# Optimization experiments

Measured on AMD Instinct MI355X. Metric: run time of the kernel, lower is better.

## Reference

```python
import jax, jax.numpy as jnp
import numpy as np

FIND_T = 0.5      # FIND_THRESHOLD
IOU_T = 0.5       # IOU_THRESHOLD
DET_T = 0.5       # DETECT_THRESHOLD
DATA_W = 416.0
DATA_H = 416.0
TOPK = 512        # fixed candidate budget for jit-compatible NMS


def _decode(out, anchors, s1, s2, case1, case2):
    # out: (B, 3*(5+C), S, S) raw head.  Faithful to get_index_and_bias +
    # get_true_position, but dense: invalid cells carried with a mask.
    B, _, S, _ = out.shape
    o = jnp.transpose(out, (0, 2, 3, 1)).reshape(B, S, S, 3, -1)  # (B,y,x,a,5+C)
    obj = jax.nn.sigmoid(o[..., 0])
    valid = obj > FIND_T
    grid = jnp.arange(S, dtype=out.dtype)
    cx = (grid[None, None, :, None] + o[..., 1]) * s1 / case1   # x index is dim 2
    cy = (grid[None, :, None, None] + o[..., 2]) * s2 / case2   # y index is dim 1
    w = jnp.exp(o[..., 3]) * anchors[:, 0] / case1              # anchors bcast over a
    h = jnp.exp(o[..., 4]) * anchors[:, 1] / case2
    cprob = jax.nn.softmax(o[..., 5:], axis=-1)
    p = obj * jnp.max(cprob, axis=-1)
    cls = jnp.argmax(cprob, axis=-1).astype(out.dtype)
    boxes = jnp.stack([p, cx, cy, w, h, cls], axis=-1).reshape(-1, 6)
    return boxes, valid.reshape(-1)


def _pairwise_iou(b):
    # b: (K,4) in (cx,cy,w,h); vectorized form of compute_iou for all pairs
    x1 = b[:, 0] - b[:, 2] / 2
    y1 = b[:, 1] - b[:, 3] / 2
    x2 = x1 + b[:, 2]
    y2 = y1 + b[:, 3]
    iw = jnp.clip(jnp.minimum(x2[:, None], x2[None, :]) - jnp.maximum(x1[:, None], x1[None, :]), 0.0)
    ih = jnp.clip(jnp.minimum(y2[:, None], y2[None, :]) - jnp.maximum(y1[:, None], y1[None, :]), 0.0)
    inter = iw * ih
    area = (x2 - x1) * (y2 - y1)
    return inter / (area[:, None] + area[None, :] - inter)


def _detect(out13, out26, out52, anchors13, anchors26, anchors52, case1, case2):
    b13, v13 = _decode(out13, anchors13, DATA_W / 13, DATA_H / 13, case1, case2)
    b26, v26 = _decode(out26, anchors26, DATA_W / 26, DATA_H / 26, case1, case2)
    b52, v52 = _decode(out52, anchors52, DATA_W / 52, DATA_H / 52, case1, case2)
    boxes = jnp.concatenate([b13, b26, b52], axis=0)
    valid = jnp.concatenate([v13, v26, v52], axis=0)

    # sort by score (descending) via fixed-size top-k over valid candidates
    score = jnp.where(valid, boxes[:, 0], -1.0)
    top_scores, idx = jax.lax.top_k(score, TOPK)
    cand = boxes[idx]                      # (K,6) sorted desc by p
    alive0 = top_scores > 0.0              # passed find-threshold
    max_p = jnp.max(jnp.where(alive0, cand[:, 0], 0.0))
    alive0 = alive0 & (cand[:, 0] > DET_T * max_p)

    iou = _pairwise_iou(cand[:, 1:5])
    same_cls = cand[:, 5][:, None] == cand[:, 5][None, :]
    # original drops all same-class boxes after a keep, and cross-class boxes
    # with iou >= threshold
    suppress_pair = same_cls | (iou >= IOU_T)
    rng = jnp.arange(TOPK)

    def body(i, state):
        suppressed, keep = state
        active = jnp.logical_not(suppressed[i])
        keep = keep.at[i].set(active)
        sup_row = active & suppress_pair[i] & (rng > i)
        return suppressed | sup_row, keep

    suppressed0 = jnp.logical_not(alive0)
    _, keep = jax.lax.fori_loop(0, TOPK, body, (suppressed0, jnp.zeros(TOPK, dtype=bool)))
    boxes_out = cand * keep[:, None].astype(cand.dtype)
    return boxes_out, keep


def setup_inputs() -> dict:
    key = jax.random.key(0)
    k1, k2, k3 = jax.random.split(key, 3)
    B, C = 32, 3 * (5 + 80)
    return {
        "out13": jax.random.normal(k1, (B, C, 13, 13), dtype=jnp.float32),
        "out26": jax.random.normal(k2, (B, C, 26, 26), dtype=jnp.float32),
        "out52": jax.random.normal(k3, (B, C, 52, 52), dtype=jnp.float32),
        "anchors13": jnp.array([[116, 90], [156, 198], [373, 326]], dtype=jnp.float32),
        "anchors26": jnp.array([[30, 61], [62, 45], [59, 119]], dtype=jnp.float32),
        "anchors52": jnp.array([[10, 13], [16, 30], [33, 23]], dtype=jnp.float32),
        "case1": jnp.float32(1.0),
        "case2": jnp.float32(1.0),
    }


def reference(out13, out26, out52, anchors13, anchors26, anchors52, case1, case2):
    return _detect(out13, out26, out52, anchors13, anchors26, anchors52, case1, case2)
```

## Files before the change

### kernel.cpp

```cpp
#include <hip/hip_runtime.h>
#include <math.h>


#define NCAND 340704
#define NCELL 113568
#define CAP   4096
#define HELEM 16
#define CELEM 4

#define OFF13 0
#define OFF26 16224
#define OFF52 81120
#define CELLS13 5408
#define CELLS26 21632

#define FIND_T 0.5f
#define IOU_T  0.5f
#define DET_T  0.5f
#define DATA_W 416.0f

#define WS_SCORES   0u
#define WS_CHIST    1362816u
#define WS_FHIST    1363840u
#define WS_COUNTER  1364864u
#define WS_KEYS     1364872u
#define WS_SKEYS    1397640u
#define WS_CAND6    1401736u
#define WS_VALID    1414024u
#define WS_MATRIX   1416072u

__device__ __forceinline__ unsigned int fmono(float f) {
    unsigned int u = __float_as_uint(f);
    return (u & 0x80000000u) ? ~u : (u | 0x80000000u);
}

__device__ int pick_bin256(unsigned int h, unsigned int need, unsigned int* above) {
    __shared__ unsigned int S[256];
    __shared__ int best; __shared__ unsigned int abv;
    int t = threadIdx.x;
    S[t] = h;
    __syncthreads();
    for (int off = 1; off < 256; off <<= 1) {
        unsigned int v = (t + off < 256) ? S[t + off] : 0u;
        __syncthreads();
        S[t] += v;
        __syncthreads();
    }
    if (t == 0) { best = 0; abv = 0; }
    __syncthreads();
    if (S[t] >= need && (t == 255 || S[t + 1] < need)) { best = t; abv = S[t] - h; }
    __syncthreads();
    if (above) *above = abv;
    return best;
}

__global__ void k_scores(const float* __restrict__ in13,
                         const float* __restrict__ in26,
                         const float* __restrict__ in52,
                         float* __restrict__ scores) {
    int cell = blockIdx.x * blockDim.x + threadIdx.x;
    if (cell >= NCELL) return;

    const float* in; int SS, b, s, candOff;
    if (cell < CELLS13) {
        in = in13; SS = 169; int l = cell;
        b = l / 169; s = l - b * 169; candOff = OFF13 + l * 3;
    } else if (cell < CELLS13 + CELLS26) {
        in = in26; SS = 676; int l = cell - CELLS13;
        b = l / 676; s = l - b * 676; candOff = OFF26 + l * 3;
    } else {
        in = in52; SS = 2704; int l = cell - (CELLS13 + CELLS26);
        b = l / 2704; s = l - b * 2704; candOff = OFF52 + l * 3;
    }

    for (int a = 0; a < 3; ++a) {
        const float* base = in + (size_t)(b * 255 + a * 85) * (size_t)SS + s;
        float o0  = base[0];
        float obj = 1.0f / (1.0f + expf(-o0));
        float vals[80];
#pragma unroll
        for (int c = 0; c < 80; ++c) vals[c] = base[(size_t)(5 + c) * (size_t)SS];
        float m = vals[0];
#pragma unroll
        for (int c = 1; c < 80; ++c) m = fmaxf(m, vals[c]);
        float sum = 0.0f;
#pragma unroll
        for (int c = 0; c < 80; ++c) sum += expf(vals[c] - m);
        float p = obj * (1.0f / sum);
        scores[candOff + a] = (obj > FIND_T) ? p : -1.0f;
    }
}

__global__ void k_hist_coarse(const float* __restrict__ scores,
                              unsigned int* __restrict__ chist) {
    __shared__ unsigned int h[256];
    int t = threadIdx.x;
    h[t] = 0;
    __syncthreads();
    int base = blockIdx.x * 256 * HELEM;
    for (int e = 0; e < HELEM; ++e) {
        int i = base + e * 256 + t;
        if (i < NCAND) atomicAdd(&h[fmono(scores[i]) >> 24], 1u);
    }
    __syncthreads();
    if (h[t]) atomicAdd(&chist[t], h[t]);
}

__global__ void k_hist_fine(const float* __restrict__ scores,
                            const unsigned int* __restrict__ chist,
                            unsigned int* __restrict__ fhist) {
    __shared__ unsigned int h[256];
    int t = threadIdx.x;
    unsigned int c = (unsigned int)pick_bin256(chist[t], 512u, 0);
    h[t] = 0;
    __syncthreads();
    int base = blockIdx.x * 256 * HELEM;
    for (int e = 0; e < HELEM; ++e) {
        int i = base + e * 256 + t;
        if (i < NCAND) {
            unsigned int mono = fmono(scores[i]);
            if ((mono >> 24) == c) atomicAdd(&h[(mono >> 16) & 0xFFu], 1u);
        }
    }
    __syncthreads();
    if (h[t]) atomicAdd(&fhist[t], h[t]);
}

__global__ void k_compact(const float* __restrict__ scores,
                          const unsigned int* __restrict__ chist,
                          const unsigned int* __restrict__ fhist,
                          unsigned int* __restrict__ counter,
                          unsigned long long* __restrict__ keys) {
    int t = threadIdx.x;
    unsigned int above;
    unsigned int c = (unsigned int)pick_bin256(chist[t], 512u, &above);
    unsigned int f = (unsigned int)pick_bin256(fhist[t], 512u - above, 0);
    unsigned int T = (c << 8) | f;

    int base = blockIdx.x * 256 * CELEM;
    for (int e = 0; e < CELEM; ++e) {
        int i = base + e * 256 + t;
        if (i < NCAND) {
            unsigned int mono = fmono(scores[i]);
            if ((mono >> 16) >= T) {
                unsigned int pos = atomicAdd(counter, 1u);
                if (pos < CAP)
                    keys[pos] = ((unsigned long long)mono << 32) |
                                (unsigned int)(~(unsigned int)i);
            }
        }
    }
}

__global__ void k_sort(const unsigned long long* __restrict__ keysg,
                       const unsigned int* __restrict__ counter,
                       unsigned long long* __restrict__ sorted) {
    __shared__ unsigned long long keys[CAP];
    int tid = threadIdx.x;
    unsigned int n = *counter; if (n > CAP) n = CAP;
    for (int t = tid; t < CAP; t += 1024)
        keys[t] = (t < (int)n) ? keysg[t] : 0ULL;
    __syncthreads();

    int sz = 1024;
    while ((unsigned)sz < n) sz <<= 1;

    for (int k = 2; k <= sz; k <<= 1) {
        for (int j = k >> 1; j > 0; j >>= 1) {
            for (int t = tid; t < (sz >> 1); t += 1024) {
                int i   = ((t & ~(j - 1)) << 1) | (t & (j - 1));
                int ixj = i | j;
                bool dir = ((i & k) == 0);
                unsigned long long x = keys[i], y = keys[ixj];
                if ((x < y) == dir) { keys[i] = y; keys[ixj] = x; }
            }
            __syncthreads();
        }
    }
    if (tid < 512) sorted[tid] = keys[tid];
}

__global__ void k_decode(const unsigned long long* __restrict__ sorted,
                         const float* __restrict__ in13,
                         const float* __restrict__ in26,
                         const float* __restrict__ in52,
                         const float* __restrict__ a13,
                         const float* __restrict__ a26,
                         const float* __restrict__ a52,
                         const float* __restrict__ c1p,
                         const float* __restrict__ c2p,
                         float* __restrict__ cand6,
                         unsigned int* __restrict__ valid) {
    int w = blockIdx.x * (blockDim.x >> 6) + (threadIdx.x >> 6);
    int lane = threadIdx.x & 63;
    if (w >= 512) return;

    unsigned long long key = sorted[w];
    int g = (int)(~(unsigned int)(key & 0xFFFFFFFFULL));

    const float* in; const float* anch; int S, SS, l;
    if (g < OFF26)      { in = in13; anch = a13; S = 13; SS = 169;  l = g - OFF13; }
    else if (g < OFF52) { in = in26; anch = a26; S = 26; SS = 676;  l = g - OFF26; }
    else                { in = in52; anch = a52; S = 52; SS = 2704; l = g - OFF52; }
    int a = l % 3; int cell = l / 3;
    int b = cell / SS; int s = cell - b * SS;
    int y = s / S; int x = s - y * S;

    const float* base = in + (size_t)(b * 255 + a * 85) * (size_t)SS + s;

    float hdr  = (lane < 5) ? base[(size_t)lane * (size_t)SS] : 0.0f;
    float val0 = base[(size_t)(5 + lane) * (size_t)SS];
    float val1 = (lane < 16) ? base[(size_t)(69 + lane) * (size_t)SS] : -INFINITY;

    float mx = fmaxf(val0, val1);
#pragma unroll
    for (int o = 32; o; o >>= 1) mx = fmaxf(mx, __shfl_xor(mx, o, 64));
    int i0 = (val0 == mx) ? lane : 1000;
    int i1 = (val1 == mx) ? lane + 64 : 1000;
    int li = i0 < i1 ? i0 : i1;
#pragma unroll
    for (int o = 32; o; o >>= 1) { int v = __shfl_xor(li, o, 64); li = v < li ? v : li; }
    float e = expf(val0 - mx) + ((lane < 16) ? expf(val1 - mx) : 0.0f);
#pragma unroll
    for (int o = 32; o; o >>= 1) e += __shfl_xor(e, o, 64);

    float o0 = __shfl(hdr, 0, 64);
    float o1 = __shfl(hdr, 1, 64);
    float o2 = __shfl(hdr, 2, 64);
    float o3 = __shfl(hdr, 3, 64);
    float o4 = __shfl(hdr, 4, 64);

    if (lane == 0) {
        float c1 = *c1p, c2 = *c2p;
        float obj = 1.0f / (1.0f + expf(-o0));
        float p = obj * (1.0f / e);
        float sgrid = DATA_W / (float)S;
        cand6[w * 6 + 0] = p;
        cand6[w * 6 + 1] = ((float)x + o1) * sgrid / c1;
        cand6[w * 6 + 2] = ((float)y + o2) * sgrid / c2;
        cand6[w * 6 + 3] = expf(o3) * anch[a * 2 + 0] / c1;
        cand6[w * 6 + 4] = expf(o4) * anch[a * 2 + 1] / c2;
        cand6[w * 6 + 5] = (float)li;
        valid[w] = ((unsigned int)(key >> 32) > 0x80000000u) ? 1u : 0u;
    }
}

__global__ void k_pairs(const float* __restrict__ cand6,
                        unsigned char* __restrict__ matrix) {
    int t = blockIdx.x * blockDim.x + threadIdx.x;
    if (t >= 512 * 64) return;
    int i = t >> 6, l = t & 63;
    float cxi = cand6[i * 6 + 1], cyi = cand6[i * 6 + 2];
    float wi  = cand6[i * 6 + 3], hi  = cand6[i * 6 + 4];
    float ci  = cand6[i * 6 + 5];
    float x1i = cxi - wi / 2.0f, y1i = cyi - hi / 2.0f;
    float x2i = x1i + wi,        y2i = y1i + hi;
    float ai  = (x2i - x1i) * (y2i - y1i);

    unsigned int byte = 0;
#pragma unroll
    for (int b = 0; b < 8; ++b) {
        int j = l * 8 + b;
        if (j > i) {
            float cxj = cand6[j * 6 + 1], cyj = cand6[j * 6 + 2];
            float wj  = cand6[j * 6 + 3], hj  = cand6[j * 6 + 4];
            float cj  = cand6[j * 6 + 5];
            bool sup = (ci == cj);
            if (!sup) {
                float x1j = cxj - wj / 2.0f, y1j = cyj - hj / 2.0f;
                float x2j = x1j + wj,        y2j = y1j + hj;
                float aj  = (x2j - x1j) * (y2j - y1j);
                float iw = fminf(x2i, x2j) - fmaxf(x1i, x1j); iw = fmaxf(iw, 0.0f);
                float ih = fminf(y2i, y2j) - fmaxf(y1i, y1j); ih = fmaxf(ih, 0.0f);
                float inter = iw * ih;
                float iou = inter / (ai + aj - inter);
                sup = (iou >= IOU_T);
            }
            byte |= ((unsigned int)sup) << b;
        }
    }
    matrix[i * 64 + l] = (unsigned char)byte;
}

__global__ void k_nms(const unsigned char* __restrict__ matrix,
                      const unsigned int* __restrict__ valid,
                      const float* __restrict__ cand6,
                      float* __restrict__ out) {
    __shared__ uint4 mbuf[2048];
    const unsigned char* m = (const unsigned char*)mbuf;
    int lane = threadIdx.x;

    const uint4* src = (const uint4*)matrix;
    for (int t = lane; t < 2048; t += 64) mbuf[t] = src[t];

    float maxp = valid[0] ? cand6[0] : 0.0f;

    unsigned int state = 0;
#pragma unroll
    for (int b = 0; b < 8; ++b) {
        int r = lane * 8 + b;
        bool alive = valid[r] && (cand6[r * 6] > DET_T * maxp);
        if (!alive) state |= 1u << b;
    }
    __syncthreads();

    unsigned int keepmask = 0;
    for (int i = 0; i < 512; ++i) {
        int srcl = i >> 3, bit = i & 7;
        unsigned int sb = (unsigned int)__shfl((int)state, srcl, 64);
        bool active = ((sb >> bit) & 1u) == 0u;
        if (lane == srcl && active) keepmask |= 1u << bit;
        if (active) state |= (unsigned int)m[i * 64 + lane];
    }

#pragma unroll
    for (int b = 0; b < 8; ++b) {
        int r = lane * 8 + b;
        float k = ((keepmask >> b) & 1u) ? 1.0f : 0.0f;
        for (int c = 0; c < 6; ++c) out[r * 6 + c] = cand6[r * 6 + c] * k;
        out[512 * 6 + r] = k;
    }
}

extern "C" void kernel_launch(void* const* d_in, const int* in_sizes, int n_in,
                              void* d_out, int out_size, void* d_ws, size_t ws_size,
                              hipStream_t stream) {
    (void)in_sizes; (void)n_in; (void)out_size; (void)ws_size;
    const float* in13 = (const float*)d_in[0];
    const float* in26 = (const float*)d_in[1];
    const float* in52 = (const float*)d_in[2];
    const float* a13  = (const float*)d_in[3];
    const float* a26  = (const float*)d_in[4];
    const float* a52  = (const float*)d_in[5];
    const float* c1p  = (const float*)d_in[6];
    const float* c2p  = (const float*)d_in[7];

    char* wsb = (char*)d_ws;
    float* scores             = (float*)(wsb + WS_SCORES);
    unsigned int* chist       = (unsigned int*)(wsb + WS_CHIST);
    unsigned int* fhist       = (unsigned int*)(wsb + WS_FHIST);
    unsigned int* counter     = (unsigned int*)(wsb + WS_COUNTER);
    unsigned long long* keys  = (unsigned long long*)(wsb + WS_KEYS);
    unsigned long long* skeys = (unsigned long long*)(wsb + WS_SKEYS);
    float* cand6              = (float*)(wsb + WS_CAND6);
    unsigned int* valid       = (unsigned int*)(wsb + WS_VALID);
    unsigned char* matrix     = (unsigned char*)(wsb + WS_MATRIX);

    hipMemsetAsync(wsb + WS_CHIST, 0, 1024 + 1024 + 8, stream);

    const int hblocks = (NCAND + 256 * HELEM - 1) / (256 * HELEM);
    const int cblocks = (NCAND + 256 * CELEM - 1) / (256 * CELEM);

    k_scores<<<(NCELL + 255) / 256, 256, 0, stream>>>(in13, in26, in52, scores);
    k_hist_coarse<<<hblocks, 256, 0, stream>>>(scores, chist);
    k_hist_fine<<<hblocks, 256, 0, stream>>>(scores, chist, fhist);
    k_compact<<<cblocks, 256, 0, stream>>>(scores, chist, fhist, counter, keys);
    k_sort<<<1, 1024, 0, stream>>>(keys, counter, skeys);
    k_decode<<<128, 256, 0, stream>>>(skeys, in13, in26, in52,
                                      a13, a26, a52, c1p, c2p, cand6, valid);
    k_pairs<<<128, 256, 0, stream>>>(cand6, matrix);
    k_nms<<<1, 64, 0, stream>>>(matrix, valid, cand6, (float*)d_out);
}
```

Before: 263.4 us.

## Fuse score computation with coarse histogram and pairwise IoU with NMS

The score kernel now builds the coarse 256-bin histogram in shared memory as it writes each score, so the separate pass that re-reads all scores goes away. The pairwise IoU matrix kernel and the serial NMS kernel are merged into one 1024-thread block that keeps candidates and the suppression matrix in LDS. This drops two launches and the global round trip for the matrix. In exchange, the IoU work now runs on a single workgroup instead of 128 blocks, so it has far less parallelism.

```diff
diff --git a/kernel.cpp b/kernel.cpp
--- a/kernel.cpp
+++ b/kernel.cpp
@@ -27,7 +27,6 @@
 #define WS_SKEYS    1397640u
 #define WS_CAND6    1401736u
 #define WS_VALID    1414024u
-#define WS_MATRIX   1416072u
 
 __device__ __forceinline__ unsigned int fmono(float f) {
     unsigned int u = __float_as_uint(f);
@@ -54,53 +53,48 @@
     return best;
 }
 
-__global__ void k_scores(const float* __restrict__ in13,
-                         const float* __restrict__ in26,
-                         const float* __restrict__ in52,
-                         float* __restrict__ scores) {
-    int cell = blockIdx.x * blockDim.x + threadIdx.x;
-    if (cell >= NCELL) return;
-
-    const float* in; int SS, b, s, candOff;
-    if (cell < CELLS13) {
-        in = in13; SS = 169; int l = cell;
-        b = l / 169; s = l - b * 169; candOff = OFF13 + l * 3;
-    } else if (cell < CELLS13 + CELLS26) {
-        in = in26; SS = 676; int l = cell - CELLS13;
-        b = l / 676; s = l - b * 676; candOff = OFF26 + l * 3;
-    } else {
-        in = in52; SS = 2704; int l = cell - (CELLS13 + CELLS26);
-        b = l / 2704; s = l - b * 2704; candOff = OFF52 + l * 3;
-    }
-
-    for (int a = 0; a < 3; ++a) {
-        const float* base = in + (size_t)(b * 255 + a * 85) * (size_t)SS + s;
-        float o0  = base[0];
-        float obj = 1.0f / (1.0f + expf(-o0));
-        float vals[80];
-#pragma unroll
-        for (int c = 0; c < 80; ++c) vals[c] = base[(size_t)(5 + c) * (size_t)SS];
-        float m = vals[0];
-#pragma unroll
-        for (int c = 1; c < 80; ++c) m = fmaxf(m, vals[c]);
-        float sum = 0.0f;
-#pragma unroll
-        for (int c = 0; c < 80; ++c) sum += expf(vals[c] - m);
-        float p = obj * (1.0f / sum);
-        scores[candOff + a] = (obj > FIND_T) ? p : -1.0f;
-    }
-}
-
-__global__ void k_hist_coarse(const float* __restrict__ scores,
+__global__ void k_scores_hist(const float* __restrict__ in13,
+                              const float* __restrict__ in26,
+                              const float* __restrict__ in52,
+                              float* __restrict__ scores,
                               unsigned int* __restrict__ chist) {
     __shared__ unsigned int h[256];
     int t = threadIdx.x;
     h[t] = 0;
     __syncthreads();
-    int base = blockIdx.x * 256 * HELEM;
-    for (int e = 0; e < HELEM; ++e) {
-        int i = base + e * 256 + t;
-        if (i < NCAND) atomicAdd(&h[fmono(scores[i]) >> 24], 1u);
+
+    int cell = blockIdx.x * blockDim.x + t;
+    if (cell < NCELL) {
+        const float* in; int SS, b, s, candOff;
+        if (cell < CELLS13) {
+            in = in13; SS = 169; int l = cell;
+            b = l / 169; s = l - b * 169; candOff = OFF13 + l * 3;
+        } else if (cell < CELLS13 + CELLS26) {
+            in = in26; SS = 676; int l = cell - CELLS13;
+            b = l / 676; s = l - b * 676; candOff = OFF26 + l * 3;
+        } else {
+            in = in52; SS = 2704; int l = cell - (CELLS13 + CELLS26);
+            b = l / 2704; s = l - b * 2704; candOff = OFF52 + l * 3;
+        }
+
+        for (int a = 0; a < 3; ++a) {
+            const float* base = in + (size_t)(b * 255 + a * 85) * (size_t)SS + s;
+            float o0  = base[0];
+            float obj = 1.0f / (1.0f + expf(-o0));
+            float vals[80];
+#pragma unroll
+            for (int c = 0; c < 80; ++c) vals[c] = base[(size_t)(5 + c) * (size_t)SS];
+            float m = vals[0];
+#pragma unroll
+            for (int c = 1; c < 80; ++c) m = fmaxf(m, vals[c]);
+            float sum = 0.0f;
+#pragma unroll
+            for (int c = 0; c < 80; ++c) sum += expf(vals[c] - m);
+            float p = obj * (1.0f / sum);
+            float sc = (obj > FIND_T) ? p : -1.0f;
+            scores[candOff + a] = sc;
+            atomicAdd(&h[fmono(sc) >> 24], 1u);
+        }
     }
     __syncthreads();
     if (h[t]) atomicAdd(&chist[t], h[t]);
@@ -245,80 +239,84 @@
     }
 }
 
-__global__ void k_pairs(const float* __restrict__ cand6,
-                        unsigned char* __restrict__ matrix) {
-    int t = blockIdx.x * blockDim.x + threadIdx.x;
-    if (t >= 512 * 64) return;
-    int i = t >> 6, l = t & 63;
-    float cxi = cand6[i * 6 + 1], cyi = cand6[i * 6 + 2];
-    float wi  = cand6[i * 6 + 3], hi  = cand6[i * 6 + 4];
-    float ci  = cand6[i * 6 + 5];
-    float x1i = cxi - wi / 2.0f, y1i = cyi - hi / 2.0f;
-    float x2i = x1i + wi,        y2i = y1i + hi;
-    float ai  = (x2i - x1i) * (y2i - y1i);
-
-    unsigned int byte = 0;
-#pragma unroll
-    for (int b = 0; b < 8; ++b) {
-        int j = l * 8 + b;
-        if (j > i) {
-            float cxj = cand6[j * 6 + 1], cyj = cand6[j * 6 + 2];
-            float wj  = cand6[j * 6 + 3], hj  = cand6[j * 6 + 4];
-            float cj  = cand6[j * 6 + 5];
-            bool sup = (ci == cj);
-            if (!sup) {
-                float x1j = cxj - wj / 2.0f, y1j = cyj - hj / 2.0f;
-                float x2j = x1j + wj,        y2j = y1j + hj;
-                float aj  = (x2j - x1j) * (y2j - y1j);
-                float iw = fminf(x2i, x2j) - fmaxf(x1i, x1j); iw = fmaxf(iw, 0.0f);
-                float ih = fminf(y2i, y2j) - fmaxf(y1i, y1j); ih = fmaxf(ih, 0.0f);
-                float inter = iw * ih;
-                float iou = inter / (ai + aj - inter);
-                sup = (iou >= IOU_T);
+__global__ __launch_bounds__(1024) void k_pairs_nms(
+        const float* __restrict__ cand6,
+        const unsigned int* __restrict__ valid,
+        float* __restrict__ out) {
+    __shared__ unsigned char m[512 * 64];
+    __shared__ float c6[512 * 6];
+    __shared__ unsigned int vbuf[512];
+    __shared__ unsigned char keepbits[64];
+    int t = threadIdx.x;
+
+    for (int i = t; i < 512 * 6; i += 1024) c6[i] = cand6[i];
+    for (int i = t; i < 512; i += 1024) vbuf[i] = valid[i];
+    __syncthreads();
+
+    for (int idx = t; idx < 512 * 64; idx += 1024) {
+        int i = idx >> 6, l = idx & 63;
+        float cxi = c6[i * 6 + 1], cyi = c6[i * 6 + 2];
+        float wi  = c6[i * 6 + 3], hi  = c6[i * 6 + 4];
+        float ci  = c6[i * 6 + 5];
+        float x1i = cxi - wi / 2.0f, y1i = cyi - hi / 2.0f;
+        float x2i = x1i + wi,        y2i = y1i + hi;
+        float ai  = (x2i - x1i) * (y2i - y1i);
+
+        unsigned int byte = 0;
+#pragma unroll
+        for (int b = 0; b < 8; ++b) {
+            int j = l * 8 + b;
+            if (j > i) {
+                float cxj = c6[j * 6 + 1], cyj = c6[j * 6 + 2];
+                float wj  = c6[j * 6 + 3], hj  = c6[j * 6 + 4];
+                float cj  = c6[j * 6 + 5];
+                bool sup = (ci == cj);
+                if (!sup) {
+                    float x1j = cxj - wj / 2.0f, y1j = cyj - hj / 2.0f;
+                    float x2j = x1j + wj,        y2j = y1j + hj;
+                    float aj  = (x2j - x1j) * (y2j - y1j);
+                    float iw = fminf(x2i, x2j) - fmaxf(x1i, x1j); iw = fmaxf(iw, 0.0f);
+                    float ih = fminf(y2i, y2j) - fmaxf(y1i, y1j); ih = fmaxf(ih, 0.0f);
+                    float inter = iw * ih;
+                    float iou = inter / (ai + aj - inter);
+                    sup = (iou >= IOU_T);
+                }
+                byte |= ((unsigned int)sup) << b;
             }
-            byte |= ((unsigned int)sup) << b;
-        }
-    }
-    matrix[i * 64 + l] = (unsigned char)byte;
-}
-
-__global__ void k_nms(const unsigned char* __restrict__ matrix,
-                      const unsigned int* __restrict__ valid,
-                      const float* __restrict__ cand6,
-                      float* __restrict__ out) {
-    __shared__ uint4 mbuf[2048];
-    const unsigned char* m = (const unsigned char*)mbuf;
-    int lane = threadIdx.x;
-
-    const uint4* src = (const uint4*)matrix;
-    for (int t = lane; t < 2048; t += 64) mbuf[t] = src[t];
-
-    float maxp = valid[0] ? cand6[0] : 0.0f;
-
-    unsigned int state = 0;
-#pragma unroll
-    for (int b = 0; b < 8; ++b) {
-        int r = lane * 8 + b;
-        bool alive = valid[r] && (cand6[r * 6] > DET_T * maxp);
-        if (!alive) state |= 1u << b;
-    }
-    __syncthreads();
-
-    unsigned int keepmask = 0;
-    for (int i = 0; i < 512; ++i) {
-        int srcl = i >> 3, bit = i & 7;
-        unsigned int sb = (unsigned int)__shfl((int)state, srcl, 64);
-        bool active = ((sb >> bit) & 1u) == 0u;
-        if (lane == srcl && active) keepmask |= 1u << bit;
-        if (active) state |= (unsigned int)m[i * 64 + lane];
-    }
-
-#pragma unroll
-    for (int b = 0; b < 8; ++b) {
-        int r = lane * 8 + b;
-        float k = ((keepmask >> b) & 1u) ? 1.0f : 0.0f;
-        for (int c = 0; c < 6; ++c) out[r * 6 + c] = cand6[r * 6 + c] * k;
-        out[512 * 6 + r] = k;
+        }
+        m[idx] = (unsigned char)byte;
+    }
+    __syncthreads();
+
+    if (t < 64) {
+        int lane = t;
+        float maxp = vbuf[0] ? c6[0] : 0.0f;
+        unsigned int state = 0;
+#pragma unroll
+        for (int b = 0; b < 8; ++b) {
+            int r = lane * 8 + b;
+            bool alive = vbuf[r] && (c6[r * 6] > DET_T * maxp);
+            if (!alive) state |= 1u << b;
+        }
+        unsigned int keepmask = 0;
+        for (int i = 0; i < 512; ++i) {
+            int srcl = i >> 3, bit = i & 7;
+            unsigned int sb = (unsigned int)__shfl((int)state, srcl, 64);
+            bool active = ((sb >> bit) & 1u) == 0u;
+            if (lane == srcl && active) keepmask |= 1u << bit;
+            if (active) state |= (unsigned int)m[i * 64 + lane];
+        }
+        keepbits[lane] = (unsigned char)keepmask;
+    }
+    __syncthreads();
+
+    for (int idx = t; idx < 512 * 6; idx += 1024) {
+        int r = idx / 6;
+        float k = ((keepbits[r >> 3] >> (r & 7)) & 1u) ? 1.0f : 0.0f;
+        out[idx] = c6[idx] * k;
+    }
+    for (int r = t; r < 512; r += 1024) {
+        out[512 * 6 + r] = ((keepbits[r >> 3] >> (r & 7)) & 1u) ? 1.0f : 0.0f;
     }
 }
 
@@ -344,20 +342,18 @@
     unsigned long long* skeys = (unsigned long long*)(wsb + WS_SKEYS);
     float* cand6              = (float*)(wsb + WS_CAND6);
     unsigned int* valid       = (unsigned int*)(wsb + WS_VALID);
-    unsigned char* matrix     = (unsigned char*)(wsb + WS_MATRIX);
 
     hipMemsetAsync(wsb + WS_CHIST, 0, 1024 + 1024 + 8, stream);
 
     const int hblocks = (NCAND + 256 * HELEM - 1) / (256 * HELEM);
     const int cblocks = (NCAND + 256 * CELEM - 1) / (256 * CELEM);
 
-    k_scores<<<(NCELL + 255) / 256, 256, 0, stream>>>(in13, in26, in52, scores);
-    k_hist_coarse<<<hblocks, 256, 0, stream>>>(scores, chist);
+    k_scores_hist<<<(NCELL + 255) / 256, 256, 0, stream>>>(in13, in26, in52,
+                                                           scores, chist);
     k_hist_fine<<<hblocks, 256, 0, stream>>>(scores, chist, fhist);
     k_compact<<<cblocks, 256, 0, stream>>>(scores, chist, fhist, counter, keys);
     k_sort<<<1, 1024, 0, stream>>>(keys, counter, skeys);
     k_decode<<<128, 256, 0, stream>>>(skeys, in13, in26, in52,
                                       a13, a26, a52, c1p, c2p, cand6, valid);
-    k_pairs<<<128, 256, 0, stream>>>(cand6, matrix);
-    k_nms<<<1, 64, 0, stream>>>(matrix, valid, cand6, (float*)d_out);
-}
+    k_pairs_nms<<<1, 1024, 0, stream>>>(cand6, valid, (float*)d_out);
+}
```

Measured after the change: 398.7 us. 51.4% more time.
